# Performance work log

Hardware: AMD Instinct MI355X
Metric: run time of the kernel (lower is better)

Reference implementation:

```python
import jax, jax.numpy as jnp
from jax import lax
import numpy as np

S, B, T = 64, 128, 32
V_SRC, V_TRG, E, HE, HD = 32000, 32000, 256, 512, 512
PAD, SOS, EOS = 0, 1, 2


def setup_inputs() -> dict:
    key = jax.random.key(0)
    ks = jax.random.split(key, 32)
    p = lambda k, sh, s=0.05: (jax.random.normal(k, sh, jnp.float32) * s)
    inp = {
        # tokens avoid PAD/SOS/EOS so src_len == S everywhere (no packing needed)
        "src": jax.random.randint(ks[0], (S, B), 3, V_SRC).astype(jnp.int32),
        "src_len": jnp.full((B,), S, dtype=jnp.int32),
        "trg": jax.random.randint(ks[1], (T, B), 3, V_TRG).astype(jnp.int32),
        # embeddings
        "emb_enc": p(ks[2], (V_SRC, E)),
        "emb_dec": p(ks[3], (V_TRG, E)),
        # encoder bidirectional GRU (torch layout: W_ih [3H, in], W_hh [3H, H])
        "Wih_f": p(ks[4], (3 * HE, E)), "Whh_f": p(ks[5], (3 * HE, HE)),
        "bih_f": p(ks[6], (3 * HE,)),  "bhh_f": p(ks[7], (3 * HE,)),
        "Wih_b": p(ks[8], (3 * HE, E)), "Whh_b": p(ks[9], (3 * HE, HE)),
        "bih_b": p(ks[10], (3 * HE,)), "bhh_b": p(ks[11], (3 * HE,)),
        # enc->dec hidden bridge: Linear(2*HE, HD)
        "W_fc": p(ks[12], (HD, 2 * HE)), "b_fc": p(ks[13], (HD,)),
        # attention: Linear(HD + 2*HE, HD) on cat(hid, enc_out), then v [HD]
        "W_attn": p(ks[14], (HD, HD + 2 * HE)), "b_attn": p(ks[15], (HD,)),
        "v_attn": p(ks[16], (HD,)),
        # decoder GRU: input cat(emb, weighted) -> E + 2*HE
        "Wih_d": p(ks[17], (3 * HD, E + 2 * HE)), "Whh_d": p(ks[18], (3 * HD, HD)),
        "bih_d": p(ks[19], (3 * HD,)), "bhh_d": p(ks[20], (3 * HD,)),
        # fc_out: Linear(HD + 2*HE + E, V)
        "W_out": p(ks[21], (V_TRG, HD + 2 * HE + E)), "b_out": p(ks[22], (V_TRG,)),
    }
    return inp


def _gru_step(W_ih, W_hh, b_ih, b_hh):
    def step(h, x):
        gi = x @ W_ih.T + b_ih
        gh = h @ W_hh.T + b_hh
        ir, iz, i_n = jnp.split(gi, 3, axis=-1)
        hr, hz, h_n = jnp.split(gh, 3, axis=-1)
        r = jax.nn.sigmoid(ir + hr)
        z = jax.nn.sigmoid(iz + hz)
        n = jnp.tanh(i_n + r * h_n)
        h2 = (1.0 - z) * n + z * h
        return h2, h2
    return step


def reference(src, src_len, trg, emb_enc, emb_dec,
              Wih_f, Whh_f, bih_f, bhh_f, Wih_b, Whh_b, bih_b, bhh_b,
              W_fc, b_fc, W_attn, b_attn, v_attn,
              Wih_d, Whh_d, bih_d, bhh_d, W_out, b_out):
    b = src.shape[1]
    he = Whh_f.shape[1]
    hd = Whh_d.shape[1]
    vocab = W_out.shape[0]
    t_len = trg.shape[0]

    # ---- encoder: bidirectional GRU ----
    emb = emb_enc[src]                               # [S, B, E]
    h0 = jnp.zeros((b, he), emb.dtype)
    hf, outs_f = lax.scan(_gru_step(Wih_f, Whh_f, bih_f, bhh_f), h0, emb)
    hb, outs_b = lax.scan(_gru_step(Wih_b, Whh_b, bih_b, bhh_b), h0, emb[::-1])
    enc_outs = jnp.concatenate([outs_f, outs_b[::-1]], axis=-1)   # [S, B, 2HE]
    hid = jnp.tanh(jnp.concatenate([hf, hb], -1) @ W_fc.T + b_fc)  # [B, HD]

    # ---- attention precompute ----
    mask = (src != PAD).T                             # [B, S]
    enc_b = enc_outs.transpose(1, 0, 2)               # [B, S, 2HE]
    W_a_h, W_a_e = W_attn[:, :hd], W_attn[:, hd:]     # split cat(hid, enc_out)
    enc_proj = jnp.einsum('bse,de->bsd', enc_b, W_a_e) + b_attn  # [B, S, HD]

    gru_d = _gru_step(Wih_d, Whh_d, bih_d, bhh_d)

    def dec_step(h, tok):
        e = emb_dec[tok]                              # [B, E]
        energy = jnp.tanh(enc_proj + (h @ W_a_h.T)[:, None, :])
        scores = jnp.einsum('bsd,d->bs', energy, v_attn)
        scores = jnp.where(mask, scores, -1e10)
        a = jax.nn.softmax(scores, axis=1)
        w = jnp.einsum('bs,bse->be', a, enc_b)        # [B, 2HE]
        h2, _ = gru_d(h, jnp.concatenate([e, w], -1))
        logits = jnp.concatenate([h2, w, e], -1) @ W_out.T + b_out
        return h2, jax.nn.log_softmax(logits, axis=1)

    # teacher forcing (tf_ratio = 1.0): decoder inputs are trg[0..T-2]
    _, logps = lax.scan(dec_step, hid, trg[:-1])      # [T-1, B, V]

    outs = jnp.zeros((t_len, b, vocab), logps.dtype).at[:, :, EOS].set(100.0)
    outs = outs.at[:t_len - 1].set(logps)
    return outs
```

## Files before the change

kernel.cpp:

```cpp
#include <hip/hip_runtime.h>
#include <cstddef>
#include <cstdint>

#define S_LEN 64
#define BATCH 128
#define T_LEN 32
#define E_DIM 256
#define VOCAB 32000
#define XDIM 1792
#define MPAD 4096

typedef unsigned short bfu;
typedef short short8 __attribute__((ext_vector_type(8)));
typedef float f32x4 __attribute__((ext_vector_type(4)));

__device__ __forceinline__ bfu f2b(float f) {
    unsigned int x = __float_as_uint(f);
    x += 0x7fffu + ((x >> 16) & 1u);
    return (bfu)(x >> 16);
}
__device__ __forceinline__ float b2f(bfu u) { return __uint_as_float(((unsigned)u) << 16); }
__device__ __forceinline__ f32x4 MFMA16(short8 a, short8 b, f32x4 c) {
    return __builtin_amdgcn_mfma_f32_16x16x32_bf16(a, b, c, 0, 0, 0);
}
__device__ __forceinline__ float sigm(float x) {
    return 1.f / (1.f + exp2f(x * -1.4426950408889634f));
}
__device__ __forceinline__ float ftanh(float x) {
    float xc = fminf(15.f, fmaxf(-15.f, x));
    float t = exp2f(xc * 2.8853900817779268f);
    return (t - 1.f) / (t + 1.f);
}

#define GLDS(gsrc, ldst)                                                       \
    __builtin_amdgcn_global_load_lds(                                          \
        (const __attribute__((address_space(1))) void*)(gsrc),                 \
        (__attribute__((address_space(3))) void*)(ldst), 16, 0, 0)

__global__ void zero_kernel(float* __restrict__ p, int n) {
    int i = blockIdx.x * 256 + threadIdx.x;
    if (i < n) p[i] = 0.f;
}

__global__ void conv_all(
    const float* __restrict__ s0, const float* __restrict__ s1,
    const float* __restrict__ s2, const float* __restrict__ s3,
    const float* __restrict__ s4, const float* __restrict__ s5,
    const float* __restrict__ s6, const float* __restrict__ s7,
    const float* __restrict__ s8,
    bfu* __restrict__ d0, bfu* __restrict__ d1, bfu* __restrict__ d2,
    bfu* __restrict__ d3, bfu* __restrict__ d4, bfu* __restrict__ d5,
    bfu* __restrict__ d6, bfu* __restrict__ d7, bfu* __restrict__ d8)
{
    int i = blockIdx.x * 256 + threadIdx.x;
    if (i >= 15941632) return;
    const float* s; bfu* d; int base;
    if      (i <   98304) { s = s0; d = d0; base = 0; }
    else if (i <  196608) { s = s1; d = d1; base = 98304; }
    else if (i <  393216) { s = s2; d = d2; base = 196608; }
    else if (i <  589824) { s = s3; d = d3; base = 393216; }
    else if (i <  720896) { s = s4; d = d4; base = 589824; }
    else if (i <  917504) { s = s5; d = d5; base = 720896; }
    else if (i < 1409024) { s = s6; d = d6; base = 917504; }
    else if (i < 1605632) { s = s7; d = d7; base = 1409024; }
    else                  { s = s8; d = d8; base = 1605632; }
    int j = i - base;
    float4 v = ((const float4*)s)[j];
    ushort4 o;
    o.x = f2b(v.x); o.y = f2b(v.y); o.z = f2b(v.z); o.w = f2b(v.w);
    ((ushort4*)d)[j] = o;
}

__global__ void transpose_wah(const float* __restrict__ W_attn, bfu* __restrict__ WahT) {
    int i = blockIdx.x * 256 + threadIdx.x;
    if (i >= 262144) return;
    int k = i >> 9, j = i & 511;
    WahT[i] = f2b(W_attn[(size_t)j * 1536 + k]);
}

__global__ void gather_emb(const float* __restrict__ table, const int* __restrict__ idx,
                           bfu* __restrict__ out, int total) {
    int i = blockIdx.x * 256 + threadIdx.x;
    if (i >= total) return;
    int row = i >> 8, k = i & 255;
    out[i] = f2b(table[(size_t)idx[row] * E_DIM + k]);
}

__global__ void gather_trg(const float* __restrict__ table, const int* __restrict__ trg,
                           bfu* __restrict__ Xb, int total) {
    int i = blockIdx.x * 256 + threadIdx.x;
    if (i >= total) return;
    int row = i >> 8, k = i & 255;
    Xb[(size_t)row * XDIM + 1536 + k] = f2b(table[(size_t)trg[row] * E_DIM + k]);
}

__global__ __launch_bounds__(256) void gemm_bf16(
    const bfu* __restrict__ A0, int lda0, const bfu* __restrict__ W0, int ldw0,
    float* __restrict__ C0, int ldc0, const float* __restrict__ bias0, int K0,
    const bfu* __restrict__ A1, int lda1, const bfu* __restrict__ W1, int ldw1,
    float* __restrict__ C1, int ldc1, const float* __restrict__ bias1, int K1,
    int act, bfu* __restrict__ Cb0)
{
    const int z = blockIdx.z;
    const bfu* A = z ? A1 : A0;
    const bfu* W = z ? W1 : W0;
    float*     C = z ? C1 : C0;
    const float* bias = z ? bias1 : bias0;
    bfu*       Cb = z ? nullptr : Cb0;
    const int lda = z ? lda1 : lda0;
    const int ldw = z ? ldw1 : ldw0;
    const int ldc = z ? ldc1 : ldc0;
    const int K   = z ? K1 : K0;

    __shared__ short lds[2][2][4096];
    const int tid  = threadIdx.x;
    const int wid  = tid >> 6, lane = tid & 63;
    const int l15  = lane & 15, lk = lane >> 4;
    const int wr   = (wid >> 1) * 64, wc = (wid & 1) * 64;
    const size_t row0 = (size_t)blockIdx.y * 128;
    const size_t col0 = (size_t)blockIdx.x * 128;

    const int r0 = tid & 127, kc0 = tid >> 7;
    const int kc1 = kc0 + 2;
    const int sb0 = (wid * 64) * 16;
    const int sb1 = (wid * 64 + 256) * 16;

    f32x4 acc[4][4];
#pragma unroll
    for (int m = 0; m < 4; ++m)
#pragma unroll
        for (int n = 0; n < 4; ++n) acc[m][n] = (f32x4){0.f, 0.f, 0.f, 0.f};

    auto stage = [&](int buf, int kt) {
        char* ba = (char*)&lds[buf][0][0];
        char* bb = (char*)&lds[buf][1][0];
        GLDS(A + (row0 + r0) * (size_t)lda + kt + kc0 * 8, ba + sb0);
        GLDS(A + (row0 + r0) * (size_t)lda + kt + kc1 * 8, ba + sb1);
        GLDS(W + (col0 + r0) * (size_t)ldw + kt + kc0 * 8, bb + sb0);
        GLDS(W + (col0 + r0) * (size_t)ldw + kt + kc1 * 8, bb + sb1);
    };

    stage(0, 0);
    __syncthreads();
    const int nk = K >> 5;
    for (int t = 0; t < nk; ++t) {
        const int buf = t & 1;
        if (t + 1 < nk) stage(buf ^ 1, (t + 1) << 5);
        short8 af[4], bf_[4];
#pragma unroll
        for (int m = 0; m < 4; ++m)
            af[m] = *(const short8*)&lds[buf][0][lk * 1024 + (wr + m * 16 + l15) * 8];
#pragma unroll
        for (int n = 0; n < 4; ++n)
            bf_[n] = *(const short8*)&lds[buf][1][lk * 1024 + (wc + n * 16 + l15) * 8];
#pragma unroll
        for (int m = 0; m < 4; ++m)
#pragma unroll
            for (int n = 0; n < 4; ++n)
                acc[m][n] = MFMA16(af[m], bf_[n], acc[m][n]);
        __syncthreads();
    }

    float bv[4];
#pragma unroll
    for (int n = 0; n < 4; ++n)
        bv[n] = bias ? bias[col0 + wc + n * 16 + l15] : 0.f;
    const size_t crow = row0 + wr + lk * 4;
#pragma unroll
    for (int m = 0; m < 4; ++m) {
#pragma unroll
        for (int q = 0; q < 4; ++q) {
            const size_t r = crow + m * 16 + q;
            float* cp = C + r * ldc + col0 + wc + l15;
            bfu*   cb = Cb ? (Cb + r * ldc + col0 + wc + l15) : nullptr;
#pragma unroll
            for (int n = 0; n < 4; ++n) {
                float v = acc[m][n][q] + bv[n];
                if (act) v = ftanh(v);
                cp[n * 16] = v;
                if (Cb) cb[n * 16] = f2b(v);
            }
        }
    }
}

__global__ __launch_bounds__(512) void gemm_big(
    const bfu* __restrict__ A, const bfu* __restrict__ W,
    float* __restrict__ C, const float* __restrict__ bias,
    bfu* __restrict__ Lb, int obf, int bx0)
{
    __shared__ short lds[2][2][8192];
    const int tid = threadIdx.x;
    const int wid = tid >> 6, lane = tid & 63;
    const int l15 = lane & 15, lk = lane >> 4;
    const int wr = (wid >> 2) * 128;
    const int wcc = (wid & 3) * 64;
    const int fid = blockIdx.x;
    const int bx = bx0 + (fid >> 4), by = fid & 15;
    const size_t row0 = (size_t)by * 256;
    const size_t col0 = (size_t)bx * 256;

    f32x4 acc[8][4];
#pragma unroll
    for (int m = 0; m < 8; ++m)
#pragma unroll
        for (int n = 0; n < 4; ++n) acc[m][n] = (f32x4){0.f, 0.f, 0.f, 0.f};

    auto stage = [&](int buf, int kt) {
        char* ba = (char*)&lds[buf][0][0];
        char* bb = (char*)&lds[buf][1][0];
#pragma unroll
        for (int it = 0; it < 2; ++it) {
            int c = it * 512 + tid;
            int kc = c >> 8, row = c & 255;
            int base = (it * 512 + wid * 64) * 16;
            GLDS(A + (row0 + row) * (size_t)XDIM + kt + kc * 8, ba + base);
            GLDS(W + (col0 + row) * (size_t)XDIM + kt + kc * 8, bb + base);
        }
    };

    stage(0, 0);
    __syncthreads();
    for (int t = 0; t < 56; ++t) {
        const int buf = t & 1;
        if (t < 55) stage(buf ^ 1, (t + 1) * 32);
        short8 af[8], bf_[4];
#pragma unroll
        for (int m = 0; m < 8; ++m)
            af[m] = *(const short8*)&lds[buf][0][lk * 2048 + (wr + m * 16 + l15) * 8];
#pragma unroll
        for (int n = 0; n < 4; ++n)
            bf_[n] = *(const short8*)&lds[buf][1][lk * 2048 + (wcc + n * 16 + l15) * 8];
#pragma unroll
        for (int m = 0; m < 8; ++m)
#pragma unroll
            for (int n = 0; n < 4; ++n)
                acc[m][n] = MFMA16(af[m], bf_[n], acc[m][n]);
        __syncthreads();
    }
    if (row0 + wr < 3968) {
        float bv[4];
#pragma unroll
        for (int n = 0; n < 4; ++n) bv[n] = bias[col0 + wcc + n * 16 + l15];
#pragma unroll
        for (int m = 0; m < 8; ++m) {
#pragma unroll
            for (int q = 0; q < 4; ++q) {
                const size_t r = row0 + wr + lk * 4 + m * 16 + q;
                if (obf) {
                    bfu* cp = Lb + r * VOCAB + col0 + wcc + l15;
#pragma unroll
                    for (int n = 0; n < 4; ++n) {
                        unsigned hb = f2b(acc[m][n][q] + bv[n]);
                        unsigned ot = (unsigned)__shfl_xor((int)hb, 1);
                        if ((lane & 1) == 0)
                            *(unsigned*)(cp + n * 16) = (hb & 0xffffu) | (ot << 16);
                    }
                } else {
                    float* cp = C + r * VOCAB + col0 + wcc + l15;
#pragma unroll
                    for (int n = 0; n < 4; ++n) cp[n * 16] = acc[m][n][q] + bv[n];
                }
            }
        }
    }
}

__global__ __launch_bounds__(256) void enc_step(
    const float* __restrict__ gi_f, const float* __restrict__ gi_b,
    const bfu* __restrict__ Whhf_b, const bfu* __restrict__ Whhb_b,
    const float* __restrict__ bhh_f, const float* __restrict__ bhh_b,
    const float* __restrict__ hin, float* __restrict__ hout,
    const bfu* __restrict__ hbin, bfu* __restrict__ hbout,
    bfu* __restrict__ encbt, int s)
{
    __shared__ short Bs[64 * 48 * 8];
    const int tid = threadIdx.x;
    const int wid = tid >> 6, lane = tid & 63;
    const int l15 = lane & 15, lk = lane >> 4;
    const int dir = blockIdx.z;
    const int u0 = blockIdx.x * 16;
    const int p = dir ? (S_LEN - 1 - s) : s;
    const bfu* Whh = dir ? Whhb_b : Whhf_b;
    const float* bhh = dir ? bhh_b : bhh_f;
    const float* gi = (dir ? gi_b : gi_f) + (size_t)p * BATCH * 1536;

    {
        char* bb = (char*)Bs;
#pragma unroll
        for (int it = 0; it < 12; ++it) {
            int c = it * 256 + tid;
            int r48 = c % 48, kc = c / 48;
            int wr = (r48 >> 4) * 512 + u0 + (r48 & 15);
            GLDS(Whh + (size_t)wr * 512 + kc * 8, bb + (it * 256 + wid * 64) * 16);
        }
    }
    __syncthreads();

    const bfu* ap0 = hbin + (size_t)(wid * 32 + l15) * 1024 + dir * 512 + lk * 8;
    const bfu* ap1 = ap0 + (size_t)16 * 1024;
    f32x4 acc[2][3];
#pragma unroll
    for (int m = 0; m < 2; ++m)
#pragma unroll
        for (int g = 0; g < 3; ++g) acc[m][g] = (f32x4){0.f, 0.f, 0.f, 0.f};

#pragma unroll
    for (int kk = 0; kk < 16; ++kk) {
        short8 a0 = *(const short8*)(ap0 + kk * 32);
        short8 a1 = *(const short8*)(ap1 + kk * 32);
#pragma unroll
        for (int g = 0; g < 3; ++g) {
            short8 bf_ = *(const short8*)&Bs[((kk * 4 + lk) * 48 + g * 16 + l15) * 8];
            acc[0][g] = MFMA16(a0, bf_, acc[0][g]);
            acc[1][g] = MFMA16(a1, bf_, acc[1][g]);
        }
    }

    const int u = u0 + l15;
    const float bR = bhh[u], bZ = bhh[512 + u], bN = bhh[1024 + u];
#pragma unroll
    for (int m = 0; m < 2; ++m) {
#pragma unroll
        for (int q = 0; q < 4; ++q) {
            const int b = wid * 32 + m * 16 + lk * 4 + q;
            const float* gib = gi + (size_t)b * 1536;
            float rr = sigm(gib[u] + acc[m][0][q] + bR);
            float zz = sigm(gib[512 + u] + acc[m][1][q] + bZ);
            float nn = ftanh(gib[1024 + u] + rr * (acc[m][2][q] + bN));
            float h2 = (1.f - zz) * nn + zz * hin[(size_t)b * 1024 + dir * 512 + u];
            hout[(size_t)b * 1024 + dir * 512 + u] = h2;
            hbout[(size_t)b * 1024 + dir * 512 + u] = f2b(h2);
            encbt[((size_t)b * S_LEN + p) * 1024 + dir * 512 + u] = f2b(h2);
        }
    }
}

__global__ __launch_bounds__(256) void attn_fused(
    const bfu* __restrict__ hb, const bfu* __restrict__ WahT,
    const float* __restrict__ encp, const bfu* __restrict__ encbt,
    const float* __restrict__ v_attn, const int* __restrict__ src,
    bfu* __restrict__ wbuf, bfu* __restrict__ Xb, int t)
{
    __shared__ float hls[512];
    __shared__ float vas[512];
    __shared__ float hps[512];
    __shared__ float sc[64];
    const int b = blockIdx.x, tid = threadIdx.x;
    for (int i = tid; i < 512; i += 256) {
        hls[i] = b2f(hb[(size_t)b * 512 + i]);
        vas[i] = v_attn[i];
    }
    __syncthreads();
    {
        const unsigned* wt = (const unsigned*)WahT;
        float a0 = 0.f, a1 = 0.f;
#pragma unroll 8
        for (int k = 0; k < 512; ++k) {
            unsigned w = wt[k * 256 + tid];
            float hk = hls[k];
            a0 += hk * __uint_as_float(w << 16);
            a1 += hk * __uint_as_float(w & 0xffff0000u);
        }
        hps[tid * 2]     = a0;
        hps[tid * 2 + 1] = a1;
    }
    __syncthreads();
    const int s = tid >> 2, l4 = tid & 3;
    const float* ep = encp + ((size_t)b * S_LEN + s) * 512;
    float part = 0.f;
#pragma unroll 4
    for (int d = l4; d < 512; d += 4) part += vas[d] * ftanh(ep[d] + hps[d]);
    part += __shfl_xor(part, 1);
    part += __shfl_xor(part, 2);
    if (l4 == 0) sc[s] = (src[s * BATCH + b] != 0) ? part : -1e10f;
    __syncthreads();
    if (tid < 64) {
        float x = sc[tid], mx = x;
        for (int o = 1; o < 64; o <<= 1) mx = fmaxf(mx, __shfl_xor(mx, o));
        float e = expf(x - mx), s2 = e;
        for (int o = 1; o < 64; o <<= 1) s2 += __shfl_xor(s2, o);
        sc[tid] = e / s2;
    }
    __syncthreads();
    bfu* xw = Xb + ((size_t)t * BATCH + b) * XDIM + 512;
#pragma unroll
    for (int c = 0; c < 4; ++c) {
        int e = tid + 256 * c;
        float a2 = 0.f;
#pragma unroll 8
        for (int s2 = 0; s2 < S_LEN; ++s2) a2 += sc[s2] * b2f(encbt[((size_t)b * S_LEN + s2) * 1024 + e]);
        bfu v = f2b(a2);
        wbuf[(size_t)b * 1024 + e] = v;
        xw[e] = v;
    }
}

__global__ __launch_bounds__(256) void dec_step(
    const float* __restrict__ gie, const bfu* __restrict__ Whhd_b,
    const bfu* __restrict__ Wihd_b, const float* __restrict__ bhh_d,
    const bfu* __restrict__ hbin, const bfu* __restrict__ wbuf,
    const float* __restrict__ hin, float* __restrict__ hout,
    bfu* __restrict__ hbout, bfu* __restrict__ Xb, int t)
{
    __shared__ short Bh[64 * 48 * 8];
    __shared__ short Bw[128 * 48 * 8];
    const int tid = threadIdx.x;
    const int wid = tid >> 6, lane = tid & 63;
    const int l15 = lane & 15, lk = lane >> 4;
    const int u0 = blockIdx.x * 16;

    {
        char* bb = (char*)Bh;
#pragma unroll
        for (int it = 0; it < 12; ++it) {
            int c = it * 256 + tid;
            int r48 = c % 48, kc = c / 48;
            int wr = (r48 >> 4) * 512 + u0 + (r48 & 15);
            GLDS(Whhd_b + (size_t)wr * 512 + kc * 8, bb + (it * 256 + wid * 64) * 16);
        }
        char* bw = (char*)Bw;
#pragma unroll
        for (int it = 0; it < 24; ++it) {
            int c = it * 256 + tid;
            int r48 = c % 48, kc = c / 48;
            int wr = (r48 >> 4) * 512 + u0 + (r48 & 15);
            GLDS(Wihd_b + (size_t)wr * 1280 + 256 + kc * 8, bw + (it * 256 + wid * 64) * 16);
        }
    }
    __syncthreads();

    f32x4 accR[2], accZ[2], accNH[2], accNW[2];
#pragma unroll
    for (int m = 0; m < 2; ++m) {
        accR[m] = (f32x4){0.f, 0.f, 0.f, 0.f};
        accZ[m] = (f32x4){0.f, 0.f, 0.f, 0.f};
        accNH[m] = (f32x4){0.f, 0.f, 0.f, 0.f};
        accNW[m] = (f32x4){0.f, 0.f, 0.f, 0.f};
    }

    {
        const bfu* ap0 = hbin + (size_t)(wid * 32 + l15) * 512 + lk * 8;
        const bfu* ap1 = ap0 + (size_t)16 * 512;
#pragma unroll
        for (int kk = 0; kk < 16; ++kk) {
            short8 a0 = *(const short8*)(ap0 + kk * 32);
            short8 a1 = *(const short8*)(ap1 + kk * 32);
            short8 br = *(const short8*)&Bh[((kk * 4 + lk) * 48 + l15) * 8];
            short8 bz = *(const short8*)&Bh[((kk * 4 + lk) * 48 + 16 + l15) * 8];
            short8 bn = *(const short8*)&Bh[((kk * 4 + lk) * 48 + 32 + l15) * 8];
            accR[0] = MFMA16(a0, br, accR[0]);
            accR[1] = MFMA16(a1, br, accR[1]);
            accZ[0] = MFMA16(a0, bz, accZ[0]);
            accZ[1] = MFMA16(a1, bz, accZ[1]);
            accNH[0] = MFMA16(a0, bn, accNH[0]);
            accNH[1] = MFMA16(a1, bn, accNH[1]);
        }
    }
    {
        const bfu* ap0 = wbuf + (size_t)(wid * 32 + l15) * 1024 + lk * 8;
        const bfu* ap1 = ap0 + (size_t)16 * 1024;
#pragma unroll
        for (int kk = 0; kk < 32; ++kk) {
            short8 a0 = *(const short8*)(ap0 + kk * 32);
            short8 a1 = *(const short8*)(ap1 + kk * 32);
            short8 br = *(const short8*)&Bw[((kk * 4 + lk) * 48 + l15) * 8];
            short8 bz = *(const short8*)&Bw[((kk * 4 + lk) * 48 + 16 + l15) * 8];
            short8 bn = *(const short8*)&Bw[((kk * 4 + lk) * 48 + 32 + l15) * 8];
            accR[0] = MFMA16(a0, br, accR[0]);
            accR[1] = MFMA16(a1, br, accR[1]);
            accZ[0] = MFMA16(a0, bz, accZ[0]);
            accZ[1] = MFMA16(a1, bz, accZ[1]);
            accNW[0] = MFMA16(a0, bn, accNW[0]);
            accNW[1] = MFMA16(a1, bn, accNW[1]);
        }
    }

    const int u = u0 + l15;
    const float bR = bhh_d[u], bZ = bhh_d[512 + u], bN = bhh_d[1024 + u];
#pragma unroll
    for (int m = 0; m < 2; ++m) {
#pragma unroll
        for (int q = 0; q < 4; ++q) {
            const int b = wid * 32 + m * 16 + lk * 4 + q;
            const float* geb = gie + ((size_t)t * BATCH + b) * 1536;
            float rr = sigm(geb[u] + accR[m][q] + bR);
            float zz = sigm(geb[512 + u] + accZ[m][q] + bZ);
            float nn = ftanh(geb[1024 + u] + accNW[m][q] + rr * (accNH[m][q] + bN));
            float h2 = (1.f - zz) * nn + zz * hin[(size_t)b * 512 + u];
            hout[(size_t)b * 512 + u] = h2;
            hbout[(size_t)b * 512 + u] = f2b(h2);
            Xb[((size_t)t * BATCH + b) * XDIM + u] = f2b(h2);
        }
    }
}

__global__ __launch_bounds__(256) void log_softmax_fill(
    const bfu* __restrict__ Lb, float* __restrict__ out, int obf)
{
    __shared__ float sm[256], ss[256];
    const int row = blockIdx.x;
    const int tid = threadIdx.x;
    float* po = out + (size_t)row * VOCAB;
    if (row >= 3968) {
        float4* p4 = (float4*)po;
        for (int i = tid; i < 8000; i += 256) {
            float4 v = {0.f, 0.f, 0.f, 0.f};
            if (i == 0) v.z = 100.f;
            p4[i] = v;
        }
        return;
    }
    float m = -3.4e38f, ssum = 0.f;
    if (obf) {
        const uint4* pb = (const uint4*)(Lb + (size_t)row * VOCAB);
        for (int i = tid; i < 4000; i += 256) {
            uint4 w = pb[i];
            float x[8];
            x[0] = __uint_as_float(w.x << 16); x[1] = __uint_as_float(w.x & 0xffff0000u);
            x[2] = __uint_as_float(w.y << 16); x[3] = __uint_as_float(w.y & 0xffff0000u);
            x[4] = __uint_as_float(w.z << 16); x[5] = __uint_as_float(w.z & 0xffff0000u);
            x[6] = __uint_as_float(w.w << 16); x[7] = __uint_as_float(w.w & 0xffff0000u);
            float mx = x[0];
#pragma unroll
            for (int j = 1; j < 8; ++j) mx = fmaxf(mx, x[j]);
            float mn = fmaxf(m, mx);
            float e = 0.f;
#pragma unroll
            for (int j = 0; j < 8; ++j) e += expf(x[j] - mn);
            ssum = ssum * expf(m - mn) + e;
            m = mn;
        }
    } else {
        const float4* p4 = (const float4*)po;
        for (int i = tid; i < 8000; i += 256) {
            float4 v = p4[i];
            float mx = fmaxf(fmaxf(v.x, v.y), fmaxf(v.z, v.w));
            float mn = fmaxf(m, mx);
            ssum = ssum * expf(m - mn) + expf(v.x - mn) + expf(v.y - mn)
                 + expf(v.z - mn) + expf(v.w - mn);
            m = mn;
        }
    }
    sm[tid] = m; ss[tid] = ssum;
    __syncthreads();
    for (int off = 128; off > 0; off >>= 1) {
        if (tid < off) {
            float m2 = sm[tid + off], s2 = ss[tid + off];
            float M = fmaxf(sm[tid], m2);
            ss[tid] = ss[tid] * expf(sm[tid] - M) + s2 * expf(m2 - M);
            sm[tid] = M;
        }
        __syncthreads();
    }
    const float lse = sm[0] + logf(ss[0]);
    if (obf) {
        const uint4* pb = (const uint4*)(Lb + (size_t)row * VOCAB);
        float4* p4 = (float4*)po;
        for (int i = tid; i < 4000; i += 256) {
            uint4 w = pb[i];
            float4 a, b4;
            a.x = __uint_as_float(w.x << 16) - lse;
            a.y = __uint_as_float(w.x & 0xffff0000u) - lse;
            a.z = __uint_as_float(w.y << 16) - lse;
            a.w = __uint_as_float(w.y & 0xffff0000u) - lse;
            b4.x = __uint_as_float(w.z << 16) - lse;
            b4.y = __uint_as_float(w.z & 0xffff0000u) - lse;
            b4.z = __uint_as_float(w.w << 16) - lse;
            b4.w = __uint_as_float(w.w & 0xffff0000u) - lse;
            p4[i * 2] = a;
            p4[i * 2 + 1] = b4;
        }
    } else {
        float4* p4 = (float4*)po;
        for (int i = tid; i < 8000; i += 256) {
            float4 v = p4[i];
            v.x -= lse; v.y -= lse; v.z -= lse; v.w -= lse;
            p4[i] = v;
        }
    }
}

extern "C" void kernel_launch(void* const* d_in, const int* in_sizes, int n_in,
                              void* d_out, int out_size, void* d_ws, size_t ws_size,
                              hipStream_t stream)
{
    const int*   src     = (const int*)d_in[0];
    const int*   trg     = (const int*)d_in[2];
    const float* emb_enc = (const float*)d_in[3];
    const float* emb_dec = (const float*)d_in[4];
    const float* Wih_f   = (const float*)d_in[5];
    const float* Whh_f   = (const float*)d_in[6];
    const float* bih_f   = (const float*)d_in[7];
    const float* bhh_f   = (const float*)d_in[8];
    const float* Wih_b   = (const float*)d_in[9];
    const float* Whh_b   = (const float*)d_in[10];
    const float* bih_b   = (const float*)d_in[11];
    const float* bhh_b   = (const float*)d_in[12];
    const float* W_fc    = (const float*)d_in[13];
    const float* b_fc    = (const float*)d_in[14];
    const float* W_attn  = (const float*)d_in[15];
    const float* b_attn  = (const float*)d_in[16];
    const float* v_attn  = (const float*)d_in[17];
    const float* Wih_d   = (const float*)d_in[18];
    const float* Whh_d   = (const float*)d_in[19];
    const float* bih_d   = (const float*)d_in[20];
    const float* bhh_d   = (const float*)d_in[21];
    const float* W_out   = (const float*)d_in[22];
    const float* b_out   = (const float*)d_in[23];
    float* out = (float*)d_out;

    char* wsb = (char*)d_ws;
    size_t off = 0;
    auto alloc = [&](size_t bytes) { void* q = wsb + off; off = (off + bytes + 255) & ~(size_t)255; return q; };
    bfu*   emb_b   = (bfu*)alloc((size_t)8192 * 256 * 2);
    bfu*   encbt_b = (bfu*)alloc((size_t)8192 * 1024 * 2);
    float* encp    = (float*)alloc((size_t)8192 * 512 * 4);
    float* gi_f    = (float*)alloc((size_t)8192 * 1536 * 4);
    float* gi_b    = (float*)alloc((size_t)8192 * 1536 * 4);
    float* gie     = (float*)alloc((size_t)3968 * 1536 * 4);
    bfu*   wbuf    = (bfu*)alloc((size_t)128 * 1024 * 2);
    float* hA      = (float*)alloc((size_t)128 * 1024 * 4);
    float* hB      = (float*)alloc((size_t)128 * 1024 * 4);
    bfu*   hbA     = (bfu*)alloc((size_t)128 * 1024 * 2);
    bfu*   hbB     = (bfu*)alloc((size_t)128 * 1024 * 2);
    float* hdA     = (float*)alloc((size_t)128 * 512 * 4);
    float* hdB     = (float*)alloc((size_t)128 * 512 * 4);
    bfu*   hdbA    = (bfu*)alloc((size_t)128 * 512 * 2);
    bfu*   hdbB    = (bfu*)alloc((size_t)128 * 512 * 2);
    bfu*   Xb      = (bfu*)alloc((size_t)MPAD * XDIM * 2);
    bfu*   Wihf_b  = (bfu*)alloc((size_t)1536 * 256 * 2);
    bfu*   Wihb_b  = (bfu*)alloc((size_t)1536 * 256 * 2);
    bfu*   Whhf_b  = (bfu*)alloc((size_t)1536 * 512 * 2);
    bfu*   Whhb_b  = (bfu*)alloc((size_t)1536 * 512 * 2);
    bfu*   Wfc_b   = (bfu*)alloc((size_t)512 * 1024 * 2);
    bfu*   Wattn_b = (bfu*)alloc((size_t)512 * 1536 * 2);
    bfu*   WahT    = (bfu*)alloc((size_t)512 * 512 * 2);
    bfu*   Wihd_b  = (bfu*)alloc((size_t)1536 * 1280 * 2);
    bfu*   Whhd_b  = (bfu*)alloc((size_t)1536 * 512 * 2);
    bfu*   Wout_b  = (bfu*)alloc((size_t)VOCAB * XDIM * 2);

    const size_t lb_bytes = (size_t)MPAD * VOCAB * 2;
    bfu* Lb = nullptr;
    if (ws_size >= off + lb_bytes + 256) Lb = (bfu*)alloc(lb_bytes);
    const int obf = (Lb != nullptr) ? 1 : 0;

    conv_all<<<(15941632 + 255) / 256, 256, 0, stream>>>(
        Wih_f, Wih_b, Whh_f, Whh_b, W_fc, W_attn, Wih_d, Whh_d, W_out,
        Wihf_b, Wihb_b, Whhf_b, Whhb_b, Wfc_b, Wattn_b, Wihd_b, Whhd_b, Wout_b);
    transpose_wah<<<1024, 256, 0, stream>>>(W_attn, WahT);

    gather_emb<<<(8192 * 256 + 255) / 256, 256, 0, stream>>>(emb_enc, src, emb_b, 8192 * 256);
    gather_trg<<<(3968 * 256 + 255) / 256, 256, 0, stream>>>(emb_dec, trg, Xb, 3968 * 256);
    zero_kernel<<<(131072 + 255) / 256, 256, 0, stream>>>(hA, 131072);
    zero_kernel<<<(65536 + 255) / 256, 256, 0, stream>>>((float*)hbA, 65536);

    gemm_bf16<<<dim3(12, 64, 2), 256, 0, stream>>>(
        emb_b, 256, Wihf_b, 256, gi_f, 1536, bih_f, 256,
        emb_b, 256, Wihb_b, 256, gi_b, 1536, bih_b, 256, 0, nullptr);
    gemm_bf16<<<dim3(12, 31, 1), 256, 0, stream>>>(
        Xb + 1536, XDIM, Wihd_b, 1280, gie, 1536, bih_d, 256,
        Xb + 1536, XDIM, Wihd_b, 1280, gie, 1536, bih_d, 256, 0, nullptr);

    for (int s = 0; s < S_LEN; ++s) {
        const float* hin  = (s & 1) ? hB : hA;
        float*       hout = (s & 1) ? hA : hB;
        const bfu*   hbin = (s & 1) ? hbB : hbA;
        bfu*         hbout = (s & 1) ? hbA : hbB;
        enc_step<<<dim3(32, 1, 2), 256, 0, stream>>>(
            gi_f, gi_b, Whhf_b, Whhb_b, bhh_f, bhh_b,
            hin, hout, hbin, hbout, encbt_b, s);
    }
    gemm_bf16<<<dim3(4, 1, 1), 256, 0, stream>>>(
        hbA, 1024, Wfc_b, 1024, hdA, 512, b_fc, 1024,
        hbA, 1024, Wfc_b, 1024, hdA, 512, b_fc, 1024, 1, hdbA);
    gemm_bf16<<<dim3(4, 64, 1), 256, 0, stream>>>(
        encbt_b, 1024, Wattn_b + 512, 1536, encp, 512, b_attn, 1024,
        encbt_b, 1024, Wattn_b + 512, 1536, encp, 512, b_attn, 1024, 0, nullptr);

    for (int t = 0; t < T_LEN - 1; ++t) {
        const float* hin  = (t & 1) ? hdB : hdA;
        float*       hout = (t & 1) ? hdA : hdB;
        const bfu*   hbin = (t & 1) ? hdbB : hdbA;
        bfu*         hbout = (t & 1) ? hdbA : hdbB;
        attn_fused<<<BATCH, 256, 0, stream>>>(hbin, WahT, encp, encbt_b,
                                              v_attn, src, wbuf, Xb, t);
        dec_step<<<32, 256, 0, stream>>>(
            gie, Whhd_b, Wihd_b, bhh_d, hbin, wbuf, hin, hout, hbout, Xb, t);
    }

    int bx0 = 0;
    for (int g = 0; g < 4; ++g) {
        int nbx = (g < 3) ? 32 : 29;
        gemm_big<<<dim3(nbx * 16, 1), 512, 0, stream>>>(Xb, Wout_b, out, b_out, Lb, obf, bx0);
        bx0 += nbx;
    }
    log_softmax_fill<<<4096, 256, 0, stream>>>(Lb, out, obf);
}
```

Measured before the change: 4.306 ms.

## Split recurrent steps over batch halves, use bf16 attention projections, merge output GEMM launches

The encoder and decoder recurrent step kernels now split the batch across a second grid dimension, which doubles the block count and gives each wave one 16-row MFMA tile instead of two. This targets low occupancy on the latency-bound sequential steps, at the cost of each block reloading its weight slice. The attention projection GEMM also writes a bf16 copy that the per-step attention kernel reads, halving its memory traffic with some precision loss. The four chunked output GEMM launches are merged into a single 2000-block launch.

```diff
diff --git a/kernel.cpp b/kernel.cpp
--- a/kernel.cpp
+++ b/kernel.cpp
@@ -187,7 +187,7 @@
 __global__ __launch_bounds__(512) void gemm_big(
     const bfu* __restrict__ A, const bfu* __restrict__ W,
     float* __restrict__ C, const float* __restrict__ bias,
-    bfu* __restrict__ Lb, int obf, int bx0)
+    bfu* __restrict__ Lb, int obf)
 {
     __shared__ short lds[2][2][8192];
     const int tid = threadIdx.x;
@@ -196,7 +196,7 @@
     const int wr = (wid >> 2) * 128;
     const int wcc = (wid & 3) * 64;
     const int fid = blockIdx.x;
-    const int bx = bx0 + (fid >> 4), by = fid & 15;
+    const int bx = fid >> 4, by = fid & 15;
     const size_t row0 = (size_t)by * 256;
     const size_t col0 = (size_t)bx * 256;
 
@@ -280,6 +280,7 @@
     const int l15 = lane & 15, lk = lane >> 4;
     const int dir = blockIdx.z;
     const int u0 = blockIdx.x * 16;
+    const int bb0 = blockIdx.y * 64;
     const int p = dir ? (S_LEN - 1 - s) : s;
     const bfu* Whh = dir ? Whhb_b : Whhf_b;
     const float* bhh = dir ? bhh_b : bhh_f;
@@ -297,48 +298,40 @@
     }
     __syncthreads();
 
-    const bfu* ap0 = hbin + (size_t)(wid * 32 + l15) * 1024 + dir * 512 + lk * 8;
-    const bfu* ap1 = ap0 + (size_t)16 * 1024;
-    f32x4 acc[2][3];
-#pragma unroll
-    for (int m = 0; m < 2; ++m)
-#pragma unroll
-        for (int g = 0; g < 3; ++g) acc[m][g] = (f32x4){0.f, 0.f, 0.f, 0.f};
+    const bfu* ap0 = hbin + (size_t)(bb0 + wid * 16 + l15) * 1024 + dir * 512 + lk * 8;
+    f32x4 acc[3];
+#pragma unroll
+    for (int g = 0; g < 3; ++g) acc[g] = (f32x4){0.f, 0.f, 0.f, 0.f};
 
 #pragma unroll
     for (int kk = 0; kk < 16; ++kk) {
         short8 a0 = *(const short8*)(ap0 + kk * 32);
-        short8 a1 = *(const short8*)(ap1 + kk * 32);
 #pragma unroll
         for (int g = 0; g < 3; ++g) {
             short8 bf_ = *(const short8*)&Bs[((kk * 4 + lk) * 48 + g * 16 + l15) * 8];
-            acc[0][g] = MFMA16(a0, bf_, acc[0][g]);
-            acc[1][g] = MFMA16(a1, bf_, acc[1][g]);
+            acc[g] = MFMA16(a0, bf_, acc[g]);
         }
     }
 
     const int u = u0 + l15;
     const float bR = bhh[u], bZ = bhh[512 + u], bN = bhh[1024 + u];
 #pragma unroll
-    for (int m = 0; m < 2; ++m) {
-#pragma unroll
-        for (int q = 0; q < 4; ++q) {
-            const int b = wid * 32 + m * 16 + lk * 4 + q;
-            const float* gib = gi + (size_t)b * 1536;
-            float rr = sigm(gib[u] + acc[m][0][q] + bR);
-            float zz = sigm(gib[512 + u] + acc[m][1][q] + bZ);
-            float nn = ftanh(gib[1024 + u] + rr * (acc[m][2][q] + bN));
-            float h2 = (1.f - zz) * nn + zz * hin[(size_t)b * 1024 + dir * 512 + u];
-            hout[(size_t)b * 1024 + dir * 512 + u] = h2;
-            hbout[(size_t)b * 1024 + dir * 512 + u] = f2b(h2);
-            encbt[((size_t)b * S_LEN + p) * 1024 + dir * 512 + u] = f2b(h2);
-        }
+    for (int q = 0; q < 4; ++q) {
+        const int b = bb0 + wid * 16 + lk * 4 + q;
+        const float* gib = gi + (size_t)b * 1536;
+        float rr = sigm(gib[u] + acc[0][q] + bR);
+        float zz = sigm(gib[512 + u] + acc[1][q] + bZ);
+        float nn = ftanh(gib[1024 + u] + rr * (acc[2][q] + bN));
+        float h2 = (1.f - zz) * nn + zz * hin[(size_t)b * 1024 + dir * 512 + u];
+        hout[(size_t)b * 1024 + dir * 512 + u] = h2;
+        hbout[(size_t)b * 1024 + dir * 512 + u] = f2b(h2);
+        encbt[((size_t)b * S_LEN + p) * 1024 + dir * 512 + u] = f2b(h2);
     }
 }
 
 __global__ __launch_bounds__(256) void attn_fused(
     const bfu* __restrict__ hb, const bfu* __restrict__ WahT,
-    const float* __restrict__ encp, const bfu* __restrict__ encbt,
+    const bfu* __restrict__ encp_b, const bfu* __restrict__ encbt,
     const float* __restrict__ v_attn, const int* __restrict__ src,
     bfu* __restrict__ wbuf, bfu* __restrict__ Xb, int t)
 {
@@ -367,10 +360,14 @@
     }
     __syncthreads();
     const int s = tid >> 2, l4 = tid & 3;
-    const float* ep = encp + ((size_t)b * S_LEN + s) * 512;
+    const unsigned* epb = (const unsigned*)(encp_b + ((size_t)b * S_LEN + s) * 512);
     float part = 0.f;
 #pragma unroll 4
-    for (int d = l4; d < 512; d += 4) part += vas[d] * ftanh(ep[d] + hps[d]);
+    for (int dp = l4; dp < 256; dp += 4) {
+        unsigned w = epb[dp];
+        part += vas[2 * dp]     * ftanh(__uint_as_float(w << 16) + hps[2 * dp]);
+        part += vas[2 * dp + 1] * ftanh(__uint_as_float(w & 0xffff0000u) + hps[2 * dp + 1]);
+    }
     part += __shfl_xor(part, 1);
     part += __shfl_xor(part, 2);
     if (l4 == 0) sc[s] = (src[s * BATCH + b] != 0) ? part : -1e10f;
@@ -409,6 +406,7 @@
     const int wid = tid >> 6, lane = tid & 63;
     const int l15 = lane & 15, lk = lane >> 4;
     const int u0 = blockIdx.x * 16;
+    const int bb0 = blockIdx.y * 64;
 
     {
         char* bb = (char*)Bh;
@@ -430,68 +428,52 @@
     }
     __syncthreads();
 
-    f32x4 accR[2], accZ[2], accNH[2], accNW[2];
-#pragma unroll
-    for (int m = 0; m < 2; ++m) {
-        accR[m] = (f32x4){0.f, 0.f, 0.f, 0.f};
-        accZ[m] = (f32x4){0.f, 0.f, 0.f, 0.f};
-        accNH[m] = (f32x4){0.f, 0.f, 0.f, 0.f};
-        accNW[m] = (f32x4){0.f, 0.f, 0.f, 0.f};
-    }
+    f32x4 accR, accZ, accNH, accNW;
+    accR = (f32x4){0.f, 0.f, 0.f, 0.f};
+    accZ = (f32x4){0.f, 0.f, 0.f, 0.f};
+    accNH = (f32x4){0.f, 0.f, 0.f, 0.f};
+    accNW = (f32x4){0.f, 0.f, 0.f, 0.f};
 
     {
-        const bfu* ap0 = hbin + (size_t)(wid * 32 + l15) * 512 + lk * 8;
-        const bfu* ap1 = ap0 + (size_t)16 * 512;
+        const bfu* ap0 = hbin + (size_t)(bb0 + wid * 16 + l15) * 512 + lk * 8;
 #pragma unroll
         for (int kk = 0; kk < 16; ++kk) {
             short8 a0 = *(const short8*)(ap0 + kk * 32);
-            short8 a1 = *(const short8*)(ap1 + kk * 32);
             short8 br = *(const short8*)&Bh[((kk * 4 + lk) * 48 + l15) * 8];
             short8 bz = *(const short8*)&Bh[((kk * 4 + lk) * 48 + 16 + l15) * 8];
             short8 bn = *(const short8*)&Bh[((kk * 4 + lk) * 48 + 32 + l15) * 8];
-            accR[0] = MFMA16(a0, br, accR[0]);
-            accR[1] = MFMA16(a1, br, accR[1]);
-            accZ[0] = MFMA16(a0, bz, accZ[0]);
-            accZ[1] = MFMA16(a1, bz, accZ[1]);
-            accNH[0] = MFMA16(a0, bn, accNH[0]);
-            accNH[1] = MFMA16(a1, bn, accNH[1]);
+            accR = MFMA16(a0, br, accR);
+            accZ = MFMA16(a0, bz, accZ);
+            accNH = MFMA16(a0, bn, accNH);
         }
     }
     {
-        const bfu* ap0 = wbuf + (size_t)(wid * 32 + l15) * 1024 + lk * 8;
-        const bfu* ap1 = ap0 + (size_t)16 * 1024;
+        const bfu* ap0 = wbuf + (size_t)(bb0 + wid * 16 + l15) * 1024 + lk * 8;
 #pragma unroll
         for (int kk = 0; kk < 32; ++kk) {
             short8 a0 = *(const short8*)(ap0 + kk * 32);
-            short8 a1 = *(const short8*)(ap1 + kk * 32);
             short8 br = *(const short8*)&Bw[((kk * 4 + lk) * 48 + l15) * 8];
             short8 bz = *(const short8*)&Bw[((kk * 4 + lk) * 48 + 16 + l15) * 8];
             short8 bn = *(const short8*)&Bw[((kk * 4 + lk) * 48 + 32 + l15) * 8];
-            accR[0] = MFMA16(a0, br, accR[0]);
-            accR[1] = MFMA16(a1, br, accR[1]);
-            accZ[0] = MFMA16(a0, bz, accZ[0]);
-            accZ[1] = MFMA16(a1, bz, accZ[1]);
-            accNW[0] = MFMA16(a0, bn, accNW[0]);
-            accNW[1] = MFMA16(a1, bn, accNW[1]);
+            accR = MFMA16(a0, br, accR);
+            accZ = MFMA16(a0, bz, accZ);
+            accNW = MFMA16(a0, bn, accNW);
         }
     }
 
     const int u = u0 + l15;
     const float bR = bhh_d[u], bZ = bhh_d[512 + u], bN = bhh_d[1024 + u];
 #pragma unroll
-    for (int m = 0; m < 2; ++m) {
-#pragma unroll
-        for (int q = 0; q < 4; ++q) {
-            const int b = wid * 32 + m * 16 + lk * 4 + q;
-            const float* geb = gie + ((size_t)t * BATCH + b) * 1536;
-            float rr = sigm(geb[u] + accR[m][q] + bR);
-            float zz = sigm(geb[512 + u] + accZ[m][q] + bZ);
-            float nn = ftanh(geb[1024 + u] + accNW[m][q] + rr * (accNH[m][q] + bN));
-            float h2 = (1.f - zz) * nn + zz * hin[(size_t)b * 512 + u];
-            hout[(size_t)b * 512 + u] = h2;
-            hbout[(size_t)b * 512 + u] = f2b(h2);
-            Xb[((size_t)t * BATCH + b) * XDIM + u] = f2b(h2);
-        }
+    for (int q = 0; q < 4; ++q) {
+        const int b = bb0 + wid * 16 + lk * 4 + q;
+        const float* geb = gie + ((size_t)t * BATCH + b) * 1536;
+        float rr = sigm(geb[u] + accR[q] + bR);
+        float zz = sigm(geb[512 + u] + accZ[q] + bZ);
+        float nn = ftanh(geb[1024 + u] + accNW[q] + rr * (accNH[q] + bN));
+        float h2 = (1.f - zz) * nn + zz * hin[(size_t)b * 512 + u];
+        hout[(size_t)b * 512 + u] = h2;
+        hbout[(size_t)b * 512 + u] = f2b(h2);
+        Xb[((size_t)t * BATCH + b) * XDIM + u] = f2b(h2);
     }
 }
 
@@ -616,6 +598,7 @@
     bfu*   emb_b   = (bfu*)alloc((size_t)8192 * 256 * 2);
     bfu*   encbt_b = (bfu*)alloc((size_t)8192 * 1024 * 2);
     float* encp    = (float*)alloc((size_t)8192 * 512 * 4);
+    bfu*   encp_b  = (bfu*)alloc((size_t)8192 * 512 * 2);
     float* gi_f    = (float*)alloc((size_t)8192 * 1536 * 4);
     float* gi_b    = (float*)alloc((size_t)8192 * 1536 * 4);
     float* gie     = (float*)alloc((size_t)3968 * 1536 * 4);
@@ -667,7 +650,7 @@
         float*       hout = (s & 1) ? hA : hB;
         const bfu*   hbin = (s & 1) ? hbB : hbA;
         bfu*         hbout = (s & 1) ? hbA : hbB;
-        enc_step<<<dim3(32, 1, 2), 256, 0, stream>>>(
+        enc_step<<<dim3(32, 2, 2), 256, 0, stream>>>(
             gi_f, gi_b, Whhf_b, Whhb_b, bhh_f, bhh_b,
             hin, hout, hbin, hbout, encbt_b, s);
     }
@@ -676,24 +659,19 @@
         hbA, 1024, Wfc_b, 1024, hdA, 512, b_fc, 1024, 1, hdbA);
     gemm_bf16<<<dim3(4, 64, 1), 256, 0, stream>>>(
         encbt_b, 1024, Wattn_b + 512, 1536, encp, 512, b_attn, 1024,
-        encbt_b, 1024, Wattn_b + 512, 1536, encp, 512, b_attn, 1024, 0, nullptr);
+        encbt_b, 1024, Wattn_b + 512, 1536, encp, 512, b_attn, 1024, 0, encp_b);
 
     for (int t = 0; t < T_LEN - 1; ++t) {
         const float* hin  = (t & 1) ? hdB : hdA;
         float*       hout = (t & 1) ? hdA : hdB;
         const bfu*   hbin = (t & 1) ? hdbB : hdbA;
         bfu*         hbout = (t & 1) ? hdbA : hdbB;
-        attn_fused<<<BATCH, 256, 0, stream>>>(hbin, WahT, encp, encbt_b,
+        attn_fused<<<BATCH, 256, 0, stream>>>(hbin, WahT, encp_b, encbt_b,
                                               v_attn, src, wbuf, Xb, t);
-        dec_step<<<32, 256, 0, stream>>>(
+        dec_step<<<dim3(32, 2), 256, 0, stream>>>(
             gie, Whhd_b, Wihd_b, bhh_d, hbin, wbuf, hin, hout, hbout, Xb, t);
     }
 
-    int bx0 = 0;
-    for (int g = 0; g < 4; ++g) {
-        int nbx = (g < 3) ? 32 : 29;
-        gemm_big<<<dim3(nbx * 16, 1), 512, 0, stream>>>(Xb, Wout_b, out, b_out, Lb, obf, bx0);
-        bx0 += nbx;
-    }
+    gemm_big<<<dim3(2000, 1), 512, 0, stream>>>(Xb, Wout_b, out, b_out, Lb, obf);
     log_softmax_fill<<<4096, 256, 0, stream>>>(Lb, out, obf);
 }
```

After: 3.754 ms. 1.15x faster.
